# Kernel optimization log

Hardware: AMD Instinct MI355X
Metric: run time of the kernel (lower is better)

Reference implementation:

```python
import jax, jax.numpy as jnp
import numpy as np

N_NODES = 21
N_ACTIONS = 256
NODE_FEAT = 128


def _gcn_norm(edge_index, n):
    # Dense normalized adjacency mirroring PyG gcn_norm with add_self_loops=True.
    row, col = edge_index[0], edge_index[1]
    A = jnp.zeros((n, n), dtype=jnp.float32).at[row, col].add(1.0)
    A = A + jnp.eye(n, dtype=jnp.float32)  # self loops appended with weight 1
    deg = A.sum(axis=0)                    # scatter-add of edge weights by col
    dinv = jnp.where(deg > 0, 1.0 / jnp.sqrt(deg), 0.0)
    # out[row] += dinv[row] * dinv[col] * x[col]  ->  A_norm = D^-1/2 A D^-1/2
    return dinv[:, None] * A * dinv[None, :]


def setup_inputs() -> dict:
    key = jax.random.key(0)
    ks = jax.random.split(key, 12)
    B = 65536
    state = jax.random.normal(ks[0], (B, N_NODES, NODE_FEAT), dtype=jnp.float32)
    edge_index = jax.random.randint(ks[1], (2, 128), 0, N_NODES, dtype=jnp.int32)

    def lin(k, fan_in, fan_out):
        s = 1.0 / np.sqrt(fan_in)
        kw, kb = jax.random.split(k)
        W = jax.random.uniform(kw, (fan_in, fan_out), jnp.float32, -s, s)
        b = jax.random.uniform(kb, (fan_out,), jnp.float32, -s, s)
        return W, b

    W1, b1 = lin(ks[2], NODE_FEAT, 21)
    W2, b2 = lin(ks[3], 21, 21)
    Wf1, bf1 = lin(ks[4], 441, 512)
    Wf2, bf2 = lin(ks[5], 512, 512)
    Wf3, bf3 = lin(ks[6], 512, N_ACTIONS)
    return {"state": state, "edge_index": edge_index,
            "W1": W1, "b1": b1, "W2": W2, "b2": b2,
            "Wf1": Wf1, "bf1": bf1, "Wf2": Wf2, "bf2": bf2,
            "Wf3": Wf3, "bf3": bf3}


def reference(state, edge_index, W1, b1, W2, b2, Wf1, bf1, Wf2, bf2, Wf3, bf3):
    A = _gcn_norm(edge_index, N_NODES)                      # [21, 21]
    # GCNConv 1: A_norm @ (X W1) + b1   (no nonlinearity between GCN layers)
    h = jnp.einsum('bnf,fh->bnh', state, W1)                # [B, 21, 21]
    h = jnp.einsum('ij,bjh->bih', A, h) + b1
    # GCNConv 2
    h = jnp.einsum('bnf,fh->bnh', h, W2)
    h = jnp.einsum('ij,bjh->bih', A, h) + b2                # [B, 21, 21]
    v = h.reshape(h.shape[0], -1)[0]                        # x.view(B,-1)[0] -> [441]
    x = jax.nn.relu(v @ Wf1 + bf1)
    x = jax.nn.relu(x @ Wf2 + bf2)
    x = jax.nn.relu(x @ Wf3 + bf3)                          # [n_actions]
    return x
```

## Files before the change

kernel.cpp:

```cpp
#include <hip/hip_runtime.h>
#include <math.h>

#define APAD 28
#define W1PAD 132

#define WS_ACC1 0
#define WS_ACC2 512
#define WS_ACC3 1024

__device__ unsigned g_arrive[64 * 16];
__device__ unsigned g_go;
__device__ unsigned g_zr;
__device__ unsigned g_cnt;

__device__ __forceinline__ float agent_load(const float* p) {
    return __hip_atomic_load(p, __ATOMIC_RELAXED, __HIP_MEMORY_SCOPE_AGENT);
}
__device__ __forceinline__ void agent_store(float* p, float v) {
    __hip_atomic_store(p, v, __ATOMIC_RELAXED, __HIP_MEMORY_SCOPE_AGENT);
}
__device__ __forceinline__ unsigned flag_load(const unsigned* p) {
    return __hip_atomic_load(p, __ATOMIC_RELAXED, __HIP_MEMORY_SCOPE_AGENT);
}
__device__ __forceinline__ void flag_store(unsigned* p, unsigned v) {
    __hip_atomic_store(p, v, __ATOMIC_RELAXED, __HIP_MEMORY_SCOPE_AGENT);
}
__device__ __forceinline__ float agent_fadd(float* p, float v) {
    return __hip_atomic_fetch_add(p, v, __ATOMIC_RELAXED, __HIP_MEMORY_SCOPE_AGENT);
}

__device__ __forceinline__ void lds_barrier() {
    asm volatile("s_waitcnt lgkmcnt(0)\n\ts_barrier" ::: "memory");
}

#define BAR_LEADER 62
__device__ __forceinline__ void grid_barrier(int blk, unsigned phase) {
    __syncthreads();
    if (blk == BAR_LEADER) {
        if (threadIdx.x < 64 && threadIdx.x != BAR_LEADER) {
            while (flag_load(&g_arrive[threadIdx.x * 16]) < phase)
                __builtin_amdgcn_s_sleep(1);
        }
        __syncthreads();
        if (threadIdx.x == 0) flag_store(&g_go, phase);
    } else {
        if (threadIdx.x == 0) {
            flag_store(&g_arrive[blk * 16], phase);
            while (flag_load(&g_go) < phase)
                __builtin_amdgcn_s_sleep(1);
        }
    }
    __syncthreads();
}

__global__ __launch_bounds__(512) void fused_kernel(
    const float* __restrict__ state,
    const int*   __restrict__ edge_index,
    const float* __restrict__ W1,
    const float* __restrict__ b1,
    const float* __restrict__ W2,
    const float* __restrict__ b2,
    const float* __restrict__ Wf1,
    const float* __restrict__ bf1,
    const float* __restrict__ Wf2,
    const float* __restrict__ bf2,
    const float* __restrict__ Wf3,
    const float* __restrict__ bf3,
    float* __restrict__ ws,
    float* __restrict__ out)
{
    const int b = blockIdx.x;
    const int t = threadIdx.x;

    const bool is_gcn = (b < 21);
    const bool do_fc2 = (b >= 21 && b < 37);
    const bool do_fc3 = (b >= 37 && b < 45);

    __shared__ float sA[21 * APAD];
    __shared__ float sX[21 * W1PAD];
    __shared__ float sW1T[21 * W1PAD];
    __shared__ float sW2T[21 * APAD];
    __shared__ float sT[21 * APAD];
    __shared__ float sG[21 * APAD];
    __shared__ float sv[441];
    __shared__ float sdeg[21];
    __shared__ float sb1[21], sb2[21];
    __shared__ float x1s[32], x2s[64];
    __shared__ unsigned sflag;

    float wf1v[21];
    if (is_gcn) {
        #pragma unroll
        for (int i = 0; i < 21; ++i) wf1v[i] = Wf1[(size_t)(21 * b + i) * 512 + t];
    }
    float wf2v[32];
    float rbf1 = 0.0f;
    if (do_fc2) {
        #pragma unroll
        for (int i = 0; i < 32; ++i) wf2v[i] = Wf2[(size_t)(32 * (b - 21) + i) * 512 + t];
        if (t < 32) rbf1 = bf1[32 * (b - 21) + t];
    }
    float wf3v[64];
    float rbf2 = 0.0f;
    if (do_fc3) {
        if (t < 256) {
            #pragma unroll
            for (int i = 0; i < 64; ++i) wf3v[i] = Wf3[(size_t)(64 * (b - 37) + i) * 256 + t];
        }
        if (t < 64) rbf2 = bf2[64 * (b - 37) + t];
    }
    const float rbf3 = bf3[t & 255];

    if (b == 63) {
        agent_store(&ws[WS_ACC1 + t], 0.0f);
        agent_store(&ws[WS_ACC2 + t], 0.0f);
        if (t < 256) agent_store(&ws[WS_ACC3 + t], 0.0f);
        __syncthreads();
        if (t == 0) flag_store(&g_zr, 1u);
    }

    if (is_gcn) {
        for (int i = t; i < 21 * APAD; i += 512) {
            sA[i] = 0.0f; sW2T[i] = 0.0f; sT[i] = 0.0f; sG[i] = 0.0f;
        }
        if (t < 21) { sdeg[t] = 1.0f; sb1[t] = b1[t]; sb2[t] = b2[t]; }
        {
            const float4* src4 = (const float4*)state;
            for (int i = t; i < 672; i += 512) {
                int n = i >> 5, fc = i & 31;
                ((float4*)&sX[n * W1PAD])[fc] = src4[i];
            }
        }
        for (int i = t; i < 2688; i += 512) {
            int f = i / 21, k = i - f * 21;
            sW1T[k * W1PAD + f] = W1[i];
        }
        for (int i = t; i < 441; i += 512) {
            int f = i / 21, k = i - f * 21;
            sW2T[k * APAD + f] = W2[i];
        }
        int er = 0, ec = 0;
        if (t < 128) { er = edge_index[t]; ec = edge_index[128 + t]; }
        lds_barrier();

        if (t < 128) {
            atomicAdd(&sA[er * APAD + ec], 1.0f);
            atomicAdd(&sdeg[ec], 1.0f);
        }
        if (t < 21) atomicAdd(&sA[t * APAD + t], 1.0f);
        if (t < 441) {
            int n = t / 21, k = t - n * 21;
            const float4* x4 = (const float4*)&sX[n * W1PAD];
            const float4* w4 = (const float4*)&sW1T[k * W1PAD];
            float s = 0.0f;
            #pragma unroll
            for (int fc = 0; fc < 32; ++fc) {
                float4 a = x4[fc], ww = w4[fc];
                s += a.x * ww.x; s += a.y * ww.y; s += a.z * ww.z; s += a.w * ww.w;
            }
            sT[k * APAD + n] = s;
        }
        lds_barrier();

        if (t < 441) {
            int r = t / 21, c = t - r * 21;
            float dr = 1.0f / sqrtf(sdeg[r]);
            float dc = 1.0f / sqrtf(sdeg[c]);
            sA[r * APAD + c] = dr * sA[r * APAD + c] * dc;
        }
        lds_barrier();

        if (t < 441) {
            int r = t / 21, k = t - r * 21;
            const float4* a4 = (const float4*)&sA[r * APAD];
            const float4* h4 = (const float4*)&sT[k * APAD];
            float s = sb1[k];
            #pragma unroll
            for (int jc = 0; jc < 6; ++jc) {
                float4 a = a4[jc], h = h4[jc];
                s += a.x * h.x; s += a.y * h.y; s += a.z * h.z; s += a.w * h.w;
            }
            sG[r * APAD + k] = s;
        }
        lds_barrier();

        if (t < 441) {
            int n = t / 21, k = t - n * 21;
            const float4* g4 = (const float4*)&sG[n * APAD];
            const float4* w4 = (const float4*)&sW2T[k * APAD];
            float s = 0.0f;
            #pragma unroll
            for (int jc = 0; jc < 6; ++jc) {
                float4 g = g4[jc], ww = w4[jc];
                s += g.x * ww.x; s += g.y * ww.y; s += g.z * ww.z; s += g.w * ww.w;
            }
            sT[k * APAD + n] = s;
        }
        lds_barrier();

        if (t < 441) {
            int r = t / 21, k = t - r * 21;
            const float4* a4 = (const float4*)&sA[r * APAD];
            const float4* h4 = (const float4*)&sT[k * APAD];
            float s = sb2[k];
            #pragma unroll
            for (int jc = 0; jc < 6; ++jc) {
                float4 a = a4[jc], h = h4[jc];
                s += a.x * h.x; s += a.y * h.y; s += a.z * h.z; s += a.w * h.w;
            }
            sv[t] = s;
        }
        if (t == 448) {
            while (flag_load(&g_zr) == 0u) __builtin_amdgcn_s_sleep(1);
        }
        lds_barrier();

        {
            float s = 0.0f;
            #pragma unroll
            for (int r = 0; r < 21; ++r) s += sv[21 * b + r] * wf1v[r];
            agent_fadd(&ws[WS_ACC1 + t], s);
        }
    }

    grid_barrier(b, 1);

    if (do_fc2) {
        if (t < 32)
            x1s[t] = fmaxf(agent_load(&ws[WS_ACC1 + 32 * (b - 21) + t]) + rbf1, 0.0f);
        lds_barrier();
        float s = 0.0f;
        #pragma unroll
        for (int j = 0; j < 32; ++j) s += x1s[j] * wf2v[j];
        agent_fadd(&ws[WS_ACC2 + t], s);
    }

    grid_barrier(b, 2);

    if (do_fc3) {
        if (t < 64)
            x2s[t] = fmaxf(agent_load(&ws[WS_ACC2 + 64 * (b - 37) + t]) + rbf2, 0.0f);
        lds_barrier();
        if (t < 256) {
            float s = 0.0f;
            #pragma unroll
            for (int j = 0; j < 64; ++j) s += x2s[j] * wf3v[j];
            agent_fadd(&ws[WS_ACC3 + t], s);
        }
    }

    __syncthreads();
    if (t == 0) {
        unsigned prev = __hip_atomic_fetch_add(&g_cnt, 1u, __ATOMIC_RELAXED,
                                               __HIP_MEMORY_SCOPE_AGENT);
        sflag = (prev == 63u) ? 1u : 0u;
    }
    __syncthreads();
    if (sflag) {
        if (t < 256) {
            float a = agent_load(&ws[WS_ACC3 + t]) + rbf3;
            out[t] = fmaxf(a, 0.0f);
        }
        if (t >= 256 && t < 320) flag_store(&g_arrive[(t - 256) * 16], 0u);
        if (t == 320) flag_store(&g_go, 0u);
        if (t == 321) flag_store(&g_zr, 0u);
        if (t == 322) flag_store(&g_cnt, 0u);
    }
}

extern "C" void kernel_launch(void* const* d_in, const int* in_sizes, int n_in,
                              void* d_out, int out_size, void* d_ws, size_t ws_size,
                              hipStream_t stream)
{
    const float* state      = (const float*)d_in[0];
    const int*   edge_index = (const int*)  d_in[1];
    const float* W1  = (const float*)d_in[2];
    const float* b1  = (const float*)d_in[3];
    const float* W2  = (const float*)d_in[4];
    const float* b2  = (const float*)d_in[5];
    const float* Wf1 = (const float*)d_in[6];
    const float* bf1 = (const float*)d_in[7];
    const float* Wf2 = (const float*)d_in[8];
    const float* bf2 = (const float*)d_in[9];
    const float* Wf3 = (const float*)d_in[10];
    const float* bf3 = (const float*)d_in[11];

    float* ws  = (float*)d_ws;
    float* out = (float*)d_out;

    fused_kernel<<<64, 512, 0, stream>>>(state, edge_index, W1, b1, W2, b2,
                                         Wf1, bf1, Wf2, bf2, Wf3, bf3, ws, out);
}
```

Baseline: 15.46 us.

## Split FC3 by output columns per block and drop final atomic-count reduction

FC3 is re-partitioned so each of the 8 blocks owns 32 output columns and reduces over all 512 inputs locally: 16 partial sums per column are combined in LDS and the block writes the final ReLU output directly. This removes the global ACC3 atomic accumulation and the last-block counter handshake at the end of the kernel. The reset of the barrier flags moves to a separate handshake after barrier 2, where every block clears its own arrival slot and bumps a counter that the leader waits on before clearing the go flag. The trade-off is that each FC3 block now reads a strided slice of Wf3 and needs two extra LDS barriers. The leader block also gains a spin-wait at the end.

```diff
diff --git a/kernel.cpp b/kernel.cpp
--- a/kernel.cpp
+++ b/kernel.cpp
@@ -6,12 +6,11 @@
 
 #define WS_ACC1 0
 #define WS_ACC2 512
-#define WS_ACC3 1024
 
 __device__ unsigned g_arrive[64 * 16];
 __device__ unsigned g_go;
 __device__ unsigned g_zr;
-__device__ unsigned g_cnt;
+__device__ unsigned g_seen;
 
 __device__ __forceinline__ float agent_load(const float* p) {
     return __hip_atomic_load(p, __ATOMIC_RELAXED, __HIP_MEMORY_SCOPE_AGENT);
@@ -24,6 +23,10 @@
 }
 __device__ __forceinline__ void flag_store(unsigned* p, unsigned v) {
     __hip_atomic_store(p, v, __ATOMIC_RELAXED, __HIP_MEMORY_SCOPE_AGENT);
+}
+__device__ __forceinline__ void flag_bump(unsigned* p) {
+    (void)__hip_atomic_fetch_add(p, 1u, __ATOMIC_RELAXED,
+                                 __HIP_MEMORY_SCOPE_AGENT);
 }
 __device__ __forceinline__ float agent_fadd(float* p, float v) {
     return __hip_atomic_fetch_add(p, v, __ATOMIC_RELAXED, __HIP_MEMORY_SCOPE_AGENT);
@@ -85,8 +88,9 @@
     __shared__ float sv[441];
     __shared__ float sdeg[21];
     __shared__ float sb1[21], sb2[21];
-    __shared__ float x1s[32], x2s[64];
-    __shared__ unsigned sflag;
+    __shared__ float x1s[32];
+    __shared__ float x2s[512];
+    __shared__ float pt[32 * 16];
 
     float wf1v[21];
     if (is_gcn) {
@@ -100,21 +104,21 @@
         for (int i = 0; i < 32; ++i) wf2v[i] = Wf2[(size_t)(32 * (b - 21) + i) * 512 + t];
         if (t < 32) rbf1 = bf1[32 * (b - 21) + t];
     }
-    float wf3v[64];
-    float rbf2 = 0.0f;
+    const int jg = t >> 5, cl = t & 31;
+    const int c0 = 32 * (b - 37);
+    float wf3v[32];
+    float rbf2 = 0.0f, rbf3r = 0.0f;
     if (do_fc3) {
-        if (t < 256) {
-            #pragma unroll
-            for (int i = 0; i < 64; ++i) wf3v[i] = Wf3[(size_t)(64 * (b - 37) + i) * 256 + t];
-        }
-        if (t < 64) rbf2 = bf2[64 * (b - 37) + t];
-    }
-    const float rbf3 = bf3[t & 255];
+        #pragma unroll
+        for (int jj = 0; jj < 32; ++jj)
+            wf3v[jj] = Wf3[(size_t)(32 * jg + jj) * 256 + c0 + cl];
+        rbf2 = bf2[t];
+        if (t < 32) rbf3r = bf3[c0 + t];
+    }
 
     if (b == 63) {
         agent_store(&ws[WS_ACC1 + t], 0.0f);
         agent_store(&ws[WS_ACC2 + t], 0.0f);
-        if (t < 256) agent_store(&ws[WS_ACC3 + t], 0.0f);
         __syncthreads();
         if (t == 0) flag_store(&g_zr, 1u);
     }
@@ -225,6 +229,8 @@
 
     grid_barrier(b, 1);
 
+    if (b == 63 && t == 0) flag_store(&g_zr, 0u);
+
     if (do_fc2) {
         if (t < 32)
             x1s[t] = fmaxf(agent_load(&ws[WS_ACC1 + 32 * (b - 21) + t]) + rbf1, 0.0f);
@@ -237,34 +243,35 @@
 
     grid_barrier(b, 2);
 
+    if (b != BAR_LEADER) {
+        if (t == 0) {
+            flag_store(&g_arrive[b * 16], 0u);
+            flag_bump(&g_seen);
+        }
+    } else {
+        if (t == 0) {
+            while (flag_load(&g_seen) < 63u) __builtin_amdgcn_s_sleep(1);
+            flag_store(&g_go, 0u);
+            flag_store(&g_seen, 0u);
+        }
+    }
+
     if (do_fc3) {
-        if (t < 64)
-            x2s[t] = fmaxf(agent_load(&ws[WS_ACC2 + 64 * (b - 37) + t]) + rbf2, 0.0f);
-        lds_barrier();
-        if (t < 256) {
-            float s = 0.0f;
-            #pragma unroll
-            for (int j = 0; j < 64; ++j) s += x2s[j] * wf3v[j];
-            agent_fadd(&ws[WS_ACC3 + t], s);
-        }
-    }
-
-    __syncthreads();
-    if (t == 0) {
-        unsigned prev = __hip_atomic_fetch_add(&g_cnt, 1u, __ATOMIC_RELAXED,
-                                               __HIP_MEMORY_SCOPE_AGENT);
-        sflag = (prev == 63u) ? 1u : 0u;
-    }
-    __syncthreads();
-    if (sflag) {
-        if (t < 256) {
-            float a = agent_load(&ws[WS_ACC3 + t]) + rbf3;
-            out[t] = fmaxf(a, 0.0f);
-        }
-        if (t >= 256 && t < 320) flag_store(&g_arrive[(t - 256) * 16], 0u);
-        if (t == 320) flag_store(&g_go, 0u);
-        if (t == 321) flag_store(&g_zr, 0u);
-        if (t == 322) flag_store(&g_cnt, 0u);
+        x2s[t] = fmaxf(agent_load(&ws[WS_ACC2 + t]) + rbf2, 0.0f);
+        lds_barrier();
+        {
+            float s = 0.0f;
+            #pragma unroll
+            for (int jj = 0; jj < 32; ++jj) s += x2s[32 * jg + jj] * wf3v[jj];
+            pt[cl * 16 + jg] = s;
+        }
+        lds_barrier();
+        if (t < 32) {
+            float s = 0.0f;
+            #pragma unroll
+            for (int g = 0; g < 16; ++g) s += pt[t * 16 + g];
+            out[c0 + t] = fmaxf(s + rbf3r, 0.0f);
+        }
     }
 }
 
```

After: 15.69 us. No clear change (+1.5%).
